# Kernel tuning notes

Hardware: AMD Instinct MI355X
Metric: run time of the kernel (lower is better)

The kernel has to match this reference:

```python
import jax, jax.numpy as jnp
import numpy as np

V, D, H, F, L, B, S = 32000, 1024, 16, 4096, 6, 2, 1024
DH = D // H


def setup_inputs() -> dict:
    key = jax.random.key(0)
    ks = jax.random.split(key, 12)
    n = lambda k, shape: jax.random.normal(k, shape, jnp.float32) * 0.02
    inp = {}
    inp['x'] = jax.random.randint(ks[0], (B, S), 0, V)
    # causal mask: 1 = masked (upper triangle), matches masked_fill(mask==1, -inf)
    inp['mask'] = jnp.triu(jnp.ones((S, S), jnp.int32), k=1)[None, None]
    inp['embed'] = n(ks[1], (V, D))
    inp['wq'] = n(ks[2], (L, D, D)); inp['bq'] = jnp.zeros((L, D), jnp.float32)
    inp['wk'] = n(ks[3], (L, D, D)); inp['bk'] = jnp.zeros((L, D), jnp.float32)
    inp['wv'] = n(ks[4], (L, D, D)); inp['bv'] = jnp.zeros((L, D), jnp.float32)
    inp['wo'] = n(ks[5], (L, D, D)); inp['bo'] = jnp.zeros((L, D), jnp.float32)
    inp['w1'] = n(ks[6], (L, D, F)); inp['b1'] = jnp.zeros((L, F), jnp.float32)
    inp['w2'] = n(ks[7], (L, F, D)); inp['b2'] = jnp.zeros((L, D), jnp.float32)
    inp['ln1_g'] = jnp.ones((L, D), jnp.float32); inp['ln1_b'] = jnp.zeros((L, D), jnp.float32)
    inp['ln2_g'] = jnp.ones((L, D), jnp.float32); inp['ln2_b'] = jnp.zeros((L, D), jnp.float32)
    inp['lnf_g'] = jnp.ones((D,), jnp.float32); inp['lnf_b'] = jnp.zeros((D,), jnp.float32)
    inp['proj_w'] = n(ks[8], (D, V)); inp['proj_b'] = jnp.zeros((V,), jnp.float32)
    return inp


def _layernorm(x, g, b, eps=1e-5):
    mu = jnp.mean(x, axis=-1, keepdims=True)
    var = jnp.var(x, axis=-1, keepdims=True)
    return (x - mu) * jax.lax.rsqrt(var + eps) * g + b


def _positional_encoding(s, d):
    pos = jnp.arange(s, dtype=jnp.float32)[:, None]
    div = jnp.exp(jnp.arange(0, d, 2, dtype=jnp.float32) * (-jnp.log(10000.0) / d))
    pe = jnp.zeros((s, d), jnp.float32)
    pe = pe.at[:, 0::2].set(jnp.sin(pos * div))
    pe = pe.at[:, 1::2].set(jnp.cos(pos * div))
    return pe


def reference(x, mask, embed, wq, bq, wk, bk, wv, bv, wo, bo, w1, b1, w2, b2,
              ln1_g, ln1_b, ln2_g, ln2_b, lnf_g, lnf_b, proj_w, proj_b):
    b_, s_ = x.shape
    h = embed[x] * jnp.sqrt(jnp.float32(D))          # [B,S,D]
    h = h + _positional_encoding(s_, D)[None]
    scale = 1.0 / jnp.sqrt(jnp.float32(DH))

    def layer(h, p):
        Wq, Bq, Wk, Bk, Wv, Bv, Wo, Bo, W1, B1, W2, B2, G1, Be1, G2, Be2 = p
        q = (h @ Wq + Bq).reshape(b_, s_, H, DH).transpose(0, 2, 1, 3)   # [B,H,S,Dh]
        k = (h @ Wk + Bk).reshape(b_, s_, H, DH).transpose(0, 2, 1, 3)
        v = (h @ Wv + Bv).reshape(b_, s_, H, DH).transpose(0, 2, 1, 3)
        scores = jnp.einsum('bhqd,bhkd->bhqk', q, k) * scale            # [B,H,S,S]
        scores = jnp.where(mask == 1, -jnp.inf, scores)
        attn = jax.nn.softmax(scores, axis=-1)
        ctx = jnp.einsum('bhqk,bhkd->bhqd', attn, v)
        ctx = ctx.transpose(0, 2, 1, 3).reshape(b_, s_, D) @ Wo + Bo
        h = _layernorm(h + ctx, G1, Be1)
        ffn = jax.nn.relu(h @ W1 + B1) @ W2 + B2
        h = _layernorm(h + ffn, G2, Be2)
        return h, None

    h, _ = jax.lax.scan(layer, h, (wq, bq, wk, bk, wv, bv, wo, bo,
                                   w1, b1, w2, b2, ln1_g, ln1_b, ln2_g, ln2_b))
    h = _layernorm(h, lnf_g, lnf_b)
    return h @ proj_w + proj_b                                           # [B,S,V]
```

## Files before the change

kernel.cpp:

```cpp
#include <hip/hip_runtime.h>
#include <math.h>

#define D_MODEL 1024
#define NHEADS 16
#define DHEAD 64
#define FDIM 4096
#define NLAYERS 6
#define BATCH 2
#define SEQ 1024
#define NROWS (BATCH*SEQ)
#define VOCAB 32000

typedef __attribute__((ext_vector_type(4))) float f32x4;
typedef __attribute__((ext_vector_type(4))) __bf16 bf16x4;
typedef __attribute__((ext_vector_type(8))) __bf16 bf16x8;

__device__ __forceinline__ void gll16(const void* g, void* l) {
  __builtin_amdgcn_global_load_lds(
      (const __attribute__((address_space(1))) unsigned int*)g,
      (__attribute__((address_space(3))) unsigned int*)l, 16, 0, 0);
}

__global__ __launch_bounds__(256) void transpose_w(
    const float* __restrict__ W, __bf16* __restrict__ Wt, int K, int N) {
  __shared__ __bf16 Ls[64][68];
  const size_t moff = (size_t)blockIdx.z * K * N;
  const float* Wl = W + moff;
  __bf16* Wtl = Wt + moff;
  const int n0 = blockIdx.x * 64, k0 = blockIdx.y * 64;
  const int tid = threadIdx.x;
  #pragma unroll
  for (int p = 0; p < 4; ++p) {
    int e = tid + p * 256;
    int r = e >> 4, c4 = (e & 15) * 4;
    float4 v = *(const float4*)&Wl[(size_t)(k0 + r) * N + n0 + c4];
    Ls[c4 + 0][r] = (__bf16)v.x; Ls[c4 + 1][r] = (__bf16)v.y;
    Ls[c4 + 2][r] = (__bf16)v.z; Ls[c4 + 3][r] = (__bf16)v.w;
  }
  __syncthreads();
  #pragma unroll
  for (int p = 0; p < 4; ++p) {
    int e = tid + p * 256;
    int r2 = e >> 4, c8 = (e & 15) * 4;
    bf16x4 o{Ls[r2][c8], Ls[r2][c8 + 1], Ls[r2][c8 + 2], Ls[r2][c8 + 3]};
    *(bf16x4*)&Wtl[(size_t)(n0 + r2) * K + k0 + c8] = o;
  }
}

struct GemmP {
  const __bf16* A;
  const __bf16* W[3];
  const float* B[3];
  void* C[3];
  int N, K;
};

template<int BM, int RELU, int OUTF32>
__global__ __launch_bounds__(256) void gemm_bf16(GemmP g) {
  constexpr int BK = 64;
  const __bf16* __restrict__ A = g.A;
  const __bf16* __restrict__ W = g.W[blockIdx.z];
  const float* __restrict__ bias = g.B[blockIdx.z];
  const int N = g.N, K = g.K;

  __shared__ __bf16 As[2][BM * BK];
  __shared__ __bf16 Bs[2][128 * BK];

  const int tid = threadIdx.x;
  const int lane = tid & 63, w = tid >> 6;

  const int gx = gridDim.x;
  const int nblk = gx * gridDim.y;
  const int id = blockIdx.x + blockIdx.y * gx;
  const int per = nblk >> 3;
  const int sid = (id & 7) * per + (id >> 3);
  const int row0 = (sid % gx) * BM;
  const int col0 = (sid / gx) * 128;

  const int wm = w >> 1, wn = w & 1;
  const int lr = lane & 15, rsw = lr & 7;

  constexpr int MI = BM / 32;
  f32x4 acc[MI][4] = {};

  const int swg = ((lane & 7) ^ (lane >> 3)) * 8;
  const __bf16* Ag = A + (size_t)(row0 + w * (BM / 4) + (lane >> 3)) * K + swg;
  const __bf16* Wg = W + (size_t)(col0 + w * 32 + (lane >> 3)) * K + swg;

  const int NT = K / BK;

  auto stage = [&](int buf, int t) {
    const int k0 = t * BK;
    #pragma unroll
    for (int s = 0; s < BM / 32; ++s)
      gll16(Ag + (size_t)s * 8 * K + k0, &As[buf][(w * (BM / 4) + s * 8) * BK]);
    #pragma unroll
    for (int s = 0; s < 4; ++s)
      gll16(Wg + (size_t)s * 8 * K + k0, &Bs[buf][(w * 32 + s * 8) * BK]);
  };

  stage(0, 0);
  __syncthreads();

  int cur = 0;
  for (int t = 0; t < NT; ++t) {
    if (t + 1 < NT) stage(cur ^ 1, t + 1);
    #pragma unroll
    for (int kk = 0; kk < 2; ++kk) {
      const int gsw = ((kk * 4 + (lane >> 4)) ^ rsw) * 8;
      bf16x8 af[MI], bf[4];
      #pragma unroll
      for (int i = 0; i < MI; ++i)
        af[i] = *(const bf16x8*)&As[cur][(wm * (BM / 2) + i * 16 + lr) * BK + gsw];
      #pragma unroll
      for (int j = 0; j < 4; ++j)
        bf[j] = *(const bf16x8*)&Bs[cur][(wn * 64 + j * 16 + lr) * BK + gsw];
      #pragma unroll
      for (int i = 0; i < MI; ++i)
        #pragma unroll
        for (int j = 0; j < 4; ++j)
          acc[i][j] = __builtin_amdgcn_mfma_f32_16x16x32_bf16(af[i], bf[j], acc[i][j], 0, 0, 0);
    }
    __syncthreads();
    cur ^= 1;
  }

  #pragma unroll
  for (int i = 0; i < MI; ++i) {
    #pragma unroll
    for (int j = 0; j < 4; ++j) {
      int col = col0 + wn * 64 + j * 16 + lr;
      float bb = bias[col];
      #pragma unroll
      for (int r = 0; r < 4; ++r) {
        int row = row0 + wm * (BM / 2) + i * 16 + (lane >> 4) * 4 + r;
        float v = acc[i][j][r] + bb;
        if (RELU) v = fmaxf(v, 0.0f);
        if (OUTF32) ((float*)g.C[blockIdx.z])[(size_t)row * N + col] = v;
        else ((__bf16*)g.C[blockIdx.z])[(size_t)row * N + col] = (__bf16)v;
      }
    }
  }
}

__global__ __launch_bounds__(256) void attn_kernel(
    const __bf16* __restrict__ Q, const __bf16* __restrict__ K,
    const __bf16* __restrict__ V, __bf16* __restrict__ O) {
  __shared__ __bf16 Ks[64 * 64];
  __shared__ __bf16 Vts[64 * 64];
  __shared__ __bf16 Psm[4][16 * 64];

  const int tid = threadIdx.x;
  const int lane = tid & 63, w = tid >> 6;
  const int q0 = blockIdx.x * 64;
  const int bh = blockIdx.y;
  const int b = bh >> 4, h = bh & 15;
  const size_t base = ((size_t)b * SEQ) * D_MODEL + (size_t)h * DHEAD;

  const int lr = lane & 15;
  const int lk = (lane >> 4) * 8;

  bf16x8 qa[2];
  {
    const __bf16* qp = Q + base + (size_t)(q0 + w * 16 + lr) * D_MODEL;
    qa[0] = *(const bf16x8*)&qp[lk];
    qa[1] = *(const bf16x8*)&qp[32 + lk];
  }

  f32x4 o_acc[4] = {};
  float m[4], l[4];
  #pragma unroll
  for (int r = 0; r < 4; ++r) { m[r] = -1e30f; l[r] = 0.0f; }

  const int nck = q0 / 64 + 1;

  for (int ck = 0; ck < nck; ++ck) {
    const int kv0 = ck * 64;
    __syncthreads();
    #pragma unroll
    for (int c = 0; c < 2; ++c) {
      int e = tid + c * 256;
      int r = e >> 3, d8 = (e & 7) * 8;
      const size_t grow = base + (size_t)(kv0 + r) * D_MODEL + d8;
      bf16x8 kv = *(const bf16x8*)&K[grow];
      *(bf16x8*)&Ks[(r * 64 + d8) ^ ((r & 7) << 3)] = kv;
      bf16x8 vv = *(const bf16x8*)&V[grow];
      #pragma unroll
      for (int j = 0; j < 8; ++j)
        Vts[((d8 + j) * 64 + r) ^ (((d8 + j) & 7) << 3)] = vv[j];
    }
    __syncthreads();

    f32x4 s_acc[4] = {};
    #pragma unroll
    for (int t = 0; t < 4; ++t) {
      int row = t * 16 + lr;
      #pragma unroll
      for (int hh = 0; hh < 2; ++hh) {
        bf16x8 kb = *(const bf16x8*)&Ks[(row * 64 + hh * 32 + lk) ^ ((row & 7) << 3)];
        s_acc[t] = __builtin_amdgcn_mfma_f32_16x16x32_bf16(qa[hh], kb, s_acc[t], 0, 0, 0);
      }
    }

    const bool diag = (ck == nck - 1);
    #pragma unroll
    for (int t = 0; t < 4; ++t) {
      int kvg = kv0 + t * 16 + lr;
      #pragma unroll
      for (int r = 0; r < 4; ++r) {
        float sv = s_acc[t][r] * 0.125f;
        if (diag) {
          int qg = q0 + w * 16 + (lane >> 4) * 4 + r;
          if (kvg > qg) sv = -1e30f;
        }
        s_acc[t][r] = sv;
      }
    }

    #pragma unroll
    for (int r = 0; r < 4; ++r) {
      float cm = fmaxf(fmaxf(s_acc[0][r], s_acc[1][r]), fmaxf(s_acc[2][r], s_acc[3][r]));
      #pragma unroll
      for (int off = 1; off < 16; off <<= 1) cm = fmaxf(cm, __shfl_xor(cm, off, 64));
      float newm = fmaxf(m[r], cm);
      float sc = __expf(m[r] - newm);
      m[r] = newm;
      float psum = 0.0f;
      #pragma unroll
      for (int t = 0; t < 4; ++t) {
        float p = __expf(s_acc[t][r] - newm);
        s_acc[t][r] = p;
        psum += p;
      }
      #pragma unroll
      for (int off = 1; off < 16; off <<= 1) psum += __shfl_xor(psum, off, 64);
      l[r] = l[r] * sc + psum;
      #pragma unroll
      for (int t = 0; t < 4; ++t) o_acc[t][r] *= sc;
    }

    #pragma unroll
    for (int t = 0; t < 4; ++t) {
      #pragma unroll
      for (int r = 0; r < 4; ++r) {
        int ql = (lane >> 4) * 4 + r;
        Psm[w][(ql * 64 + t * 16 + lr) ^ ((ql & 7) << 3)] = (__bf16)(s_acc[t][r]);
      }
    }

    bf16x8 pa[2];
    #pragma unroll
    for (int hh = 0; hh < 2; ++hh)
      pa[hh] = *(const bf16x8*)&Psm[w][(lr * 64 + hh * 32 + lk) ^ ((lr & 7) << 3)];
    #pragma unroll
    for (int t = 0; t < 4; ++t) {
      int row = t * 16 + lr;
      #pragma unroll
      for (int hh = 0; hh < 2; ++hh) {
        bf16x8 vb = *(const bf16x8*)&Vts[(row * 64 + hh * 32 + lk) ^ ((row & 7) << 3)];
        o_acc[t] = __builtin_amdgcn_mfma_f32_16x16x32_bf16(pa[hh], vb, o_acc[t], 0, 0, 0);
      }
    }
  }

  #pragma unroll
  for (int r = 0; r < 4; ++r) {
    float inv = 1.0f / l[r];
    int qg = q0 + w * 16 + (lane >> 4) * 4 + r;
    #pragma unroll
    for (int t = 0; t < 4; ++t)
      O[base + (size_t)qg * D_MODEL + t * 16 + lr] = (__bf16)(o_acc[t][r] * inv);
  }
}

template<int HASRES>
__global__ __launch_bounds__(256) void addln_kernel(
    const __bf16* __restrict__ X, const __bf16* __restrict__ Rr,
    const float* __restrict__ g, const float* __restrict__ bb,
    __bf16* __restrict__ Out) {
  const int row = blockIdx.x;
  const int tid = threadIdx.x;
  const size_t rb = (size_t)row * D_MODEL + tid * 4;
  bf16x4 xv = *(const bf16x4*)&X[rb];
  float v[4];
  float s = 0.0f, ss = 0.0f;
  if (HASRES) {
    bf16x4 rv = *(const bf16x4*)&Rr[rb];
    #pragma unroll
    for (int i = 0; i < 4; ++i) {
      v[i] = (float)xv[i] + (float)rv[i];
      s += v[i]; ss += v[i] * v[i];
    }
  } else {
    #pragma unroll
    for (int i = 0; i < 4; ++i) { v[i] = (float)xv[i]; s += v[i]; ss += v[i] * v[i]; }
  }
  #pragma unroll
  for (int off = 32; off; off >>= 1) { s += __shfl_xor(s, off, 64); ss += __shfl_xor(ss, off, 64); }
  __shared__ float red[8];
  const int lane = tid & 63, w = tid >> 6;
  if (lane == 0) { red[w] = s; red[4 + w] = ss; }
  __syncthreads();
  s = red[0] + red[1] + red[2] + red[3];
  ss = red[4] + red[5] + red[6] + red[7];
  float mean = s * (1.0f / D_MODEL);
  float var = ss * (1.0f / D_MODEL) - mean * mean;
  float rs = rsqrtf(var + 1e-5f);
  const int d0 = tid * 4;
  bf16x4 ov;
  #pragma unroll
  for (int i = 0; i < 4; ++i)
    ov[i] = (__bf16)((v[i] - mean) * rs * g[d0 + i] + bb[d0 + i]);
  *(bf16x4*)&Out[rb] = ov;
}

__global__ __launch_bounds__(256) void embed_kernel(
    const int* __restrict__ x, const float* __restrict__ embed,
    __bf16* __restrict__ H) {
  const int row = blockIdx.x;
  const int spos = row & (SEQ - 1);
  const int tok = x[row];
  const int tid = threadIdx.x;
  const int d0 = tid * 4;
  float4 e4 = *(const float4*)&embed[(size_t)tok * D_MODEL + d0];
  float ev[4] = {e4.x, e4.y, e4.z, e4.w};
  bf16x4 ov;
  #pragma unroll
  for (int i = 0; i < 4; ++i) {
    int d = d0 + i;
    float div = expf((float)(2 * (d >> 1)) * (-9.2103403719761836f / (float)D_MODEL));
    float ang = (float)spos * div;
    float pe = (d & 1) ? cosf(ang) : sinf(ang);
    ov[i] = (__bf16)(ev[i] * 32.0f + pe);
  }
  *(bf16x4*)&H[(size_t)row * D_MODEL + d0] = ov;
}

extern "C" void kernel_launch(void* const* d_in, const int* in_sizes, int n_in,
                              void* d_out, int out_size, void* d_ws, size_t ws_size,
                              hipStream_t stream) {
  const int* x = (const int*)d_in[0];
  const float* embed = (const float*)d_in[2];
  const float* wq = (const float*)d_in[3];
  const float* bq = (const float*)d_in[4];
  const float* wk = (const float*)d_in[5];
  const float* bk = (const float*)d_in[6];
  const float* wv = (const float*)d_in[7];
  const float* bv = (const float*)d_in[8];
  const float* wo = (const float*)d_in[9];
  const float* bo = (const float*)d_in[10];
  const float* w1 = (const float*)d_in[11];
  const float* b1 = (const float*)d_in[12];
  const float* w2 = (const float*)d_in[13];
  const float* b2 = (const float*)d_in[14];
  const float* ln1g = (const float*)d_in[15];
  const float* ln1b = (const float*)d_in[16];
  const float* ln2g = (const float*)d_in[17];
  const float* ln2b = (const float*)d_in[18];
  const float* lnfg = (const float*)d_in[19];
  const float* lnfb = (const float*)d_in[20];
  const float* pw = (const float*)d_in[21];
  const float* pb = (const float*)d_in[22];
  float* out = (float*)d_out;

  char* wsp = (char*)d_ws;
  size_t off = 0;
  auto alloc = [&](size_t bytes) {
    void* p = wsp + off; off = (off + bytes + 255) & ~(size_t)255; return p;
  };
  const size_t RD2 = (size_t)NROWS * D_MODEL * 2;
  __bf16* Xb   = (__bf16*)alloc(RD2);
  __bf16* Qb   = (__bf16*)alloc(RD2);
  __bf16* Kb   = (__bf16*)alloc(RD2);
  __bf16* Vb   = (__bf16*)alloc(RD2);
  __bf16* CTXb = (__bf16*)alloc(RD2);
  __bf16* Tb   = (__bf16*)alloc(RD2);
  __bf16* H1b  = (__bf16*)alloc(RD2);
  __bf16* FFb  = Qb;
  const size_t DD = (size_t)D_MODEL * D_MODEL;
  const size_t DF = (size_t)D_MODEL * FDIM;
  __bf16* wqt = (__bf16*)alloc(NLAYERS * DD * 2);
  __bf16* wkt = (__bf16*)alloc(NLAYERS * DD * 2);
  __bf16* wvt = (__bf16*)alloc(NLAYERS * DD * 2);
  __bf16* wot = (__bf16*)alloc(NLAYERS * DD * 2);
  __bf16* w1t = (__bf16*)alloc(NLAYERS * DF * 2);
  __bf16* w2t = (__bf16*)alloc(NLAYERS * DF * 2);
  __bf16* pwt = (__bf16*)alloc((size_t)D_MODEL * VOCAB * 2);

  transpose_w<<<dim3(16, 16, NLAYERS), 256, 0, stream>>>(wq, wqt, D_MODEL, D_MODEL);
  transpose_w<<<dim3(16, 16, NLAYERS), 256, 0, stream>>>(wk, wkt, D_MODEL, D_MODEL);
  transpose_w<<<dim3(16, 16, NLAYERS), 256, 0, stream>>>(wv, wvt, D_MODEL, D_MODEL);
  transpose_w<<<dim3(16, 16, NLAYERS), 256, 0, stream>>>(wo, wot, D_MODEL, D_MODEL);
  transpose_w<<<dim3(64, 16, NLAYERS), 256, 0, stream>>>(w1, w1t, D_MODEL, FDIM);
  transpose_w<<<dim3(16, 64, NLAYERS), 256, 0, stream>>>(w2, w2t, FDIM, D_MODEL);
  transpose_w<<<dim3(500, 16, 1), 256, 0, stream>>>(pw, pwt, D_MODEL, VOCAB);

  embed_kernel<<<NROWS, 256, 0, stream>>>(x, embed, Xb);

  for (int l = 0; l < NLAYERS; ++l) {
    GemmP g{};
    g.A = Xb; g.N = D_MODEL; g.K = D_MODEL;
    g.W[0] = wqt + l * DD; g.W[1] = wkt + l * DD; g.W[2] = wvt + l * DD;
    g.B[0] = bq + l * D_MODEL; g.B[1] = bk + l * D_MODEL; g.B[2] = bv + l * D_MODEL;
    g.C[0] = Qb; g.C[1] = Kb; g.C[2] = Vb;
    gemm_bf16<128, 0, 0><<<dim3(NROWS / 128, D_MODEL / 128, 3), 256, 0, stream>>>(g);

    attn_kernel<<<dim3(SEQ / 64, BATCH * NHEADS), 256, 0, stream>>>(Qb, Kb, Vb, CTXb);

    GemmP go{};
    go.A = CTXb; go.N = D_MODEL; go.K = D_MODEL;
    go.W[0] = wot + l * DD; go.B[0] = bo + l * D_MODEL; go.C[0] = Tb;
    gemm_bf16<64, 0, 0><<<dim3(NROWS / 64, D_MODEL / 128, 1), 256, 0, stream>>>(go);

    addln_kernel<1><<<NROWS, 256, 0, stream>>>(Xb, Tb, ln1g + l * D_MODEL, ln1b + l * D_MODEL, H1b);

    GemmP g1{};
    g1.A = H1b; g1.N = FDIM; g1.K = D_MODEL;
    g1.W[0] = w1t + l * DF; g1.B[0] = b1 + l * FDIM; g1.C[0] = FFb;
    gemm_bf16<128, 1, 0><<<dim3(NROWS / 128, FDIM / 128, 1), 256, 0, stream>>>(g1);

    GemmP g2{};
    g2.A = FFb; g2.N = D_MODEL; g2.K = FDIM;
    g2.W[0] = w2t + l * DF; g2.B[0] = b2 + l * D_MODEL; g2.C[0] = Tb;
    gemm_bf16<64, 0, 0><<<dim3(NROWS / 64, D_MODEL / 128, 1), 256, 0, stream>>>(g2);

    addln_kernel<1><<<NROWS, 256, 0, stream>>>(H1b, Tb, ln2g + l * D_MODEL, ln2b + l * D_MODEL, Xb);
  }

  addln_kernel<0><<<NROWS, 256, 0, stream>>>(Xb, nullptr, lnfg, lnfb, H1b);

  GemmP gp{};
  gp.A = H1b; gp.N = VOCAB; gp.K = D_MODEL;
  gp.W[0] = pwt; gp.B[0] = pb; gp.C[0] = out;
  gemm_bf16<128, 0, 1><<<dim3(NROWS / 128, VOCAB / 128, 1), 256, 0, stream>>>(gp);
}
```

Baseline: 1.585 ms.

## Use dedicated 256x256-tile GEMM with grouped block swizzle for vocab projection

Adds a 512-thread GEMM kernel with 256x256 output tiles, double-buffered 128KB dynamic LDS, XOR-swizzled global-to-LDS loads, and a block-id remap that groups neighbouring tiles for L2 reuse. It replaces the 128-tile generic GEMM for the final vocabulary projection. The larger tile raises arithmetic intensity per LDS load and cuts redundant global traffic. In exchange it keeps one block per CU with many accumulator registers, and the id remap assumes the block count divides by 8 (125*8 blocks, which holds here).

```diff
diff --git a/kernel.cpp b/kernel.cpp
--- a/kernel.cpp
+++ b/kernel.cpp
@@ -138,6 +138,90 @@
         if (RELU) v = fmaxf(v, 0.0f);
         if (OUTF32) ((float*)g.C[blockIdx.z])[(size_t)row * N + col] = v;
         else ((__bf16*)g.C[blockIdx.z])[(size_t)row * N + col] = (__bf16)v;
+      }
+    }
+  }
+}
+
+__global__ __launch_bounds__(512, 1) void gemm_256(
+    const __bf16* __restrict__ A, const __bf16* __restrict__ W,
+    const float* __restrict__ bias, float* __restrict__ C, int N, int K) {
+  extern __shared__ __bf16 sm[];
+  __bf16* As = sm;
+  __bf16* Bs = sm + 2 * 256 * 64;
+
+  const int tid = threadIdx.x;
+  const int lane = tid & 63, w = tid >> 6;
+
+  const int gx = gridDim.x;
+  const int nblk = gx * gridDim.y;
+  const int id = blockIdx.x + blockIdx.y * gx;
+  const int per = nblk >> 3;
+  const int sid = (id & 7) * per + (id >> 3);
+  const int row0 = (sid % gx) * 256;
+  const int col0 = (sid / gx) * 256;
+
+  const int wr = w >> 2, wc = w & 3;
+  const int lr = lane & 15;
+
+  f32x4 acc[8][4] = {};
+
+  const int swg = ((lane & 7) ^ (lane >> 3)) * 8;
+  const __bf16* Ag = A + (size_t)(row0 + w * 32 + (lane >> 3)) * K + swg;
+  const __bf16* Wg = W + (size_t)(col0 + w * 32 + (lane >> 3)) * K + swg;
+
+  const int NT = K / 64;
+
+  auto stage = [&](int buf, int t) {
+    const int k0 = t * 64;
+    #pragma unroll
+    for (int s = 0; s < 4; ++s) {
+      gll16(Ag + (size_t)(s * 8) * K + k0, &As[buf * 16384 + (w * 32 + s * 8) * 64]);
+      gll16(Wg + (size_t)(s * 8) * K + k0, &Bs[buf * 16384 + (w * 32 + s * 8) * 64]);
+    }
+  };
+
+  stage(0, 0);
+  __syncthreads();
+
+  int cur = 0;
+  for (int t = 0; t < NT; ++t) {
+    if (t + 1 < NT) stage(cur ^ 1, t + 1);
+    #pragma unroll
+    for (int kk = 0; kk < 2; ++kk) {
+      bf16x8 af[8], bf[4];
+      #pragma unroll
+      for (int i = 0; i < 8; ++i) {
+        int row = wr * 128 + i * 16 + lr;
+        af[i] = *(const bf16x8*)&As[cur * 16384 + row * 64 +
+                                    (((kk * 4 + (lane >> 4)) ^ (row & 7)) * 8)];
+      }
+      #pragma unroll
+      for (int j = 0; j < 4; ++j) {
+        int row = wc * 64 + j * 16 + lr;
+        bf[j] = *(const bf16x8*)&Bs[cur * 16384 + row * 64 +
+                                    (((kk * 4 + (lane >> 4)) ^ (row & 7)) * 8)];
+      }
+      #pragma unroll
+      for (int i = 0; i < 8; ++i)
+        #pragma unroll
+        for (int j = 0; j < 4; ++j)
+          acc[i][j] = __builtin_amdgcn_mfma_f32_16x16x32_bf16(af[i], bf[j], acc[i][j], 0, 0, 0);
+    }
+    __syncthreads();
+    cur ^= 1;
+  }
+
+  #pragma unroll
+  for (int i = 0; i < 8; ++i) {
+    #pragma unroll
+    for (int j = 0; j < 4; ++j) {
+      int col = col0 + wc * 64 + j * 16 + lr;
+      float bb = bias[col];
+      #pragma unroll
+      for (int r = 0; r < 4; ++r) {
+        int row = row0 + wr * 128 + i * 16 + (lane >> 4) * 4 + r;
+        C[(size_t)row * N + col] = acc[i][j][r] + bb;
       }
     }
   }
@@ -429,8 +513,12 @@
 
   addln_kernel<0><<<NROWS, 256, 0, stream>>>(Xb, nullptr, lnfg, lnfb, H1b);
 
-  GemmP gp{};
-  gp.A = H1b; gp.N = VOCAB; gp.K = D_MODEL;
-  gp.W[0] = pwt; gp.B[0] = pb; gp.C[0] = out;
-  gemm_bf16<128, 0, 1><<<dim3(NROWS / 128, VOCAB / 128, 1), 256, 0, stream>>>(gp);
-}
+  static int lds_attr_set = 0;
+  if (!lds_attr_set) {
+    hipFuncSetAttribute((const void*)gemm_256,
+                        hipFuncAttributeMaxDynamicSharedMemorySize, 131072);
+    lds_attr_set = 1;
+  }
+  gemm_256<<<dim3(NROWS / 256, VOCAB / 256), 512, 131072, stream>>>(
+      H1b, pwt, pb, out, VOCAB, D_MODEL);
+}
```

After: 1.511 ms. 4.7% less time.
